# Optimization experiments

Measured on AMD Instinct MI355X. Metric: run time of the kernel, lower is better.

## Reference

```python
import jax, jax.numpy as jnp
import numpy as np
import math

B, S, D_MODEL, N_HEAD = 4, 2048, 1024, 16
D_K = D_MODEL // N_HEAD
ROPE_THETA = 10000.0


def _rope(x):
    # x: [B, H, S, Dk]; interleaved-pair rotary embedding.
    b, h, s, d = x.shape
    inv_freq = ROPE_THETA ** (-jnp.arange(0, d, 2, dtype=jnp.float32) / d)  # [d/2]
    ang = jnp.arange(s, dtype=jnp.float32)[:, None] * inv_freq[None, :]      # [S, d/2]
    cos, sin = jnp.cos(ang), jnp.sin(ang)
    x1, x2 = x[..., 0::2], x[..., 1::2]
    r1 = x1 * cos - x2 * sin
    r2 = x1 * sin + x2 * cos
    return jnp.stack([r1, r2], axis=-1).reshape(b, h, s, d)


def setup_inputs() -> dict:
    key = jax.random.key(0)
    ks = jax.random.split(key, 7)
    sc = 1.0 / math.sqrt(D_MODEL)
    return {
        "q": jax.random.normal(ks[0], (B, S, D_MODEL), jnp.float32),
        "k": jax.random.normal(ks[1], (B, S, D_MODEL), jnp.float32),
        "v": jax.random.normal(ks[2], (B, S, D_MODEL), jnp.float32),
        "Wq": jax.random.normal(ks[3], (D_MODEL, D_MODEL), jnp.float32) * sc,
        "Wk": jax.random.normal(ks[4], (D_MODEL, D_MODEL), jnp.float32) * sc,
        "Wv": jax.random.normal(ks[5], (D_MODEL, D_MODEL), jnp.float32) * sc,
        "Wo": jax.random.normal(ks[6], (D_MODEL, D_MODEL), jnp.float32) * sc,
    }


def _split(x):
    b, s, d = x.shape
    return x.reshape(b, s, N_HEAD, d // N_HEAD).transpose(0, 2, 1, 3)  # [B,H,S,Dk]


def reference(q, k, v, Wq, Wk, Wv, Wo):
    q = jnp.einsum("bsd,de->bse", q, Wq)
    k = jnp.einsum("bsd,de->bse", k, Wk)
    v = jnp.einsum("bsd,de->bse", v, Wv)
    qh, kh, vh = _split(q), _split(k), _split(v)
    qh, kh = _rope(qh), _rope(kh)
    scale = 1.0 / math.sqrt(D_K)
    score = jnp.einsum("bhqd,bhkd->bhqk", qh, kh) * scale  # [B,H,S,S]
    attn = jax.nn.softmax(score, axis=-1)
    out = jnp.einsum("bhqk,bhkd->bhqd", attn, vh)
    out = out.transpose(0, 2, 1, 3).reshape(q.shape[0], q.shape[1], D_MODEL)
    return jnp.einsum("bsd,de->bse", out, Wo)
```

## Files before the change

kernel.cpp:

```cpp
#include <hip/hip_runtime.h>
#include <stdint.h>

#define Bv 4
#define Sv 2048
#define Dv 1024
#define Hv 16
#define DKv 64
#define BSv (Bv * Sv)

typedef unsigned short u16;
typedef __attribute__((ext_vector_type(8))) short short8;
typedef __attribute__((ext_vector_type(8))) unsigned short u16x8;
typedef __attribute__((ext_vector_type(4))) unsigned short u16x4;
typedef __attribute__((ext_vector_type(4))) float f32x4;
typedef __attribute__((ext_vector_type(16))) float f32x16;

__device__ __forceinline__ u16 f2bf(float f) {
  union { float f; uint32_t u; } x; x.f = f;
  uint32_t r = x.u + 0x7FFFu + ((x.u >> 16) & 1u);
  return (u16)(r >> 16);
}

__device__ __forceinline__ void gl_lds16(const void* g, void* l) {
  __builtin_amdgcn_global_load_lds(
      (__attribute__((address_space(1))) void*)g,
      (__attribute__((address_space(3))) void*)l, 16, 0, 0);
}

__device__ __forceinline__ f32x4 mfma16(short8 a, short8 b, f32x4 c) {
  return __builtin_amdgcn_mfma_f32_16x16x32_bf16(a, b, c, 0, 0, 0);
}
__device__ __forceinline__ f32x16 mfma32(short8 a, short8 b, f32x16 c) {
  return __builtin_amdgcn_mfma_f32_32x32x16_bf16(a, b, c, 0, 0, 0);
}

__global__ __launch_bounds__(256) void conv_qkv(
    const float* __restrict__ q, const float* __restrict__ k,
    const float* __restrict__ v, u16* __restrict__ qb, u16* __restrict__ kb,
    u16* __restrict__ vb) {
  const float* src = (blockIdx.y == 0) ? q : (blockIdx.y == 1 ? k : v);
  u16* dst = (blockIdx.y == 0) ? qb : (blockIdx.y == 1 ? kb : vb);
  int i = (blockIdx.x * 256 + threadIdx.x) * 8;
  const float4* s4 = (const float4*)(src + i);
  float4 a = s4[0], b = s4[1];
  u16x8 o = { f2bf(a.x), f2bf(a.y), f2bf(a.z), f2bf(a.w),
              f2bf(b.x), f2bf(b.y), f2bf(b.z), f2bf(b.w) };
  *(u16x8*)(dst + i) = o;
}

__global__ __launch_bounds__(256) void conv_wt(
    const float* __restrict__ w0, const float* __restrict__ w1,
    const float* __restrict__ w2, const float* __restrict__ w3,
    u16* __restrict__ t0, u16* __restrict__ t1, u16* __restrict__ t2,
    u16* __restrict__ t3) {
  const float* W = (blockIdx.z == 0) ? w0 : (blockIdx.z == 1 ? w1 : (blockIdx.z == 2 ? w2 : w3));
  u16* T = (blockIdx.z == 0) ? t0 : (blockIdx.z == 1 ? t1 : (blockIdx.z == 2 ? t2 : t3));
  __shared__ u16 tile[64][72];
  int nb = blockIdx.x * 64, kb = blockIdx.y * 64;
  int t = threadIdx.x;
#pragma unroll
  for (int p = 0; p < 4; ++p) {
    int idx = p * 256 + t;
    int r = idx >> 4;
    int c4 = (idx & 15) * 4;
    float4 vv = *(const float4*)(W + (size_t)(kb + r) * Dv + nb + c4);
    tile[c4 + 0][r] = f2bf(vv.x);
    tile[c4 + 1][r] = f2bf(vv.y);
    tile[c4 + 2][r] = f2bf(vv.z);
    tile[c4 + 3][r] = f2bf(vv.w);
  }
  __syncthreads();
#pragma unroll
  for (int p = 0; p < 4; ++p) {
    int idx = p * 256 + t;
    int r = idx >> 4;
    int c4 = (idx & 15) * 4;
    u16x4 o = { tile[r][c4], tile[r][c4 + 1], tile[r][c4 + 2], tile[r][c4 + 3] };
    *(u16x4*)(T + (size_t)(nb + r) * Dv + kb + c4) = o;
  }
}

__global__ __launch_bounds__(256) void gemm_bt(
    const u16* __restrict__ A, const u16* __restrict__ Bt,
    void* __restrict__ Out, int mode) {
  __shared__ u16 As[128 * 64];
  __shared__ u16 Bs[128 * 64];
  int tid = threadIdx.x;
  int lane = tid & 63, wid = tid >> 6;
  int quad = lane >> 4, cc = lane & 15;
  int wm = (wid >> 1) * 64, wn = (wid & 1) * 64;
  int m0 = blockIdx.x * 128, n0 = blockIdx.y * 128;

  f32x4 acc[4][4];
#pragma unroll
  for (int mi = 0; mi < 4; ++mi)
#pragma unroll
    for (int ni = 0; ni < 4; ++ni) {
      f32x4 z = {0.f, 0.f, 0.f, 0.f};
      acc[mi][ni] = z;
    }

  for (int k0 = 0; k0 < Dv; k0 += 64) {
#pragma unroll
    for (int p = 0; p < 4; ++p) {
      int slot = p * 256 + tid;
      int row = slot >> 3, cl = slot & 7;
      int cg = cl ^ (row & 7);
      gl_lds16(A + (size_t)(m0 + row) * Dv + k0 + cg * 8, &As[slot * 8]);
    }
#pragma unroll
    for (int p = 0; p < 4; ++p) {
      int slot = p * 256 + tid;
      int row = slot >> 3, cl = slot & 7;
      int cg = cl ^ (row & 7);
      gl_lds16(Bt + (size_t)(n0 + row) * Dv + k0 + cg * 8, &Bs[slot * 8]);
    }
    __syncthreads();
#pragma unroll
    for (int kk = 0; kk < 2; ++kk) {
      short8 af[4], bf[4];
#pragma unroll
      for (int mi = 0; mi < 4; ++mi) {
        int row = wm + mi * 16 + cc;
        int cg = kk * 4 + quad;
        af[mi] = *(const short8*)&As[row * 64 + (cg ^ (row & 7)) * 8];
      }
#pragma unroll
      for (int ni = 0; ni < 4; ++ni) {
        int row = wn + ni * 16 + cc;
        int cg = kk * 4 + quad;
        bf[ni] = *(const short8*)&Bs[row * 64 + (cg ^ (row & 7)) * 8];
      }
#pragma unroll
      for (int mi = 0; mi < 4; ++mi)
#pragma unroll
        for (int ni = 0; ni < 4; ++ni)
          acc[mi][ni] = mfma16(af[mi], bf[ni], acc[mi][ni]);
    }
    __syncthreads();
  }

  if (mode <= 1) {
    u16* O = (u16*)Out;
    float postscale = (mode == 0) ? 0.18033688011112042f : 1.0f;
#pragma unroll
    for (int ni = 0; ni < 4; ++ni) {
      int n = n0 + wn + ni * 16 + cc;
      int h = n >> 6, d = n & 63;
      float inv = __expf(-(float)(d & 62) * (9.210340372f / 64.0f));
      float sign = (d & 1) ? 1.0f : -1.0f;
#pragma unroll
      for (int mi = 0; mi < 4; ++mi) {
        int mB = m0 + wm + mi * 16 + quad * 4;
#pragma unroll
        for (int r = 0; r < 4; ++r) {
          int m = mB + r;
          int b = m >> 11, s = m & (Sv - 1);
          float val = acc[mi][ni][r];
          float part = __shfl_xor(val, 1);
          float sn, cs;
          __sincosf((float)s * inv, &sn, &cs);
          float outv = (val * cs + sign * part * sn) * postscale;
          O[((size_t)(b * Hv + h) * Sv + s) * DKv + d] = f2bf(outv);
        }
      }
    }
  } else if (mode == 2) {
    u16* O = (u16*)Out;
#pragma unroll
    for (int ni = 0; ni < 4; ++ni) {
      int n = n0 + wn + ni * 16 + cc;
      int h = n >> 6, d = n & 63;
#pragma unroll
      for (int mi = 0; mi < 4; ++mi) {
        int mB = m0 + wm + mi * 16 + quad * 4;
        int b = mB >> 11, s = mB & (Sv - 1);
        u16x4 o4 = { f2bf(acc[mi][ni][0]), f2bf(acc[mi][ni][1]),
                     f2bf(acc[mi][ni][2]), f2bf(acc[mi][ni][3]) };
        *(u16x4*)&O[((size_t)(b * Hv + h) * DKv + d) * Sv + s] = o4;
      }
    }
  } else {
    float* O = (float*)Out;
#pragma unroll
    for (int ni = 0; ni < 4; ++ni) {
      int n = n0 + wn + ni * 16 + cc;
#pragma unroll
      for (int mi = 0; mi < 4; ++mi) {
        int mB = m0 + wm + mi * 16 + quad * 4;
#pragma unroll
        for (int r = 0; r < 4; ++r)
          O[(size_t)(mB + r) * Dv + n] = acc[mi][ni][r];
      }
    }
  }
}

__global__ __launch_bounds__(256, 2) void attn(
    const u16* __restrict__ Qp, const u16* __restrict__ Kp,
    const u16* __restrict__ Vt, u16* __restrict__ ctx) {
  __shared__ u16 Ks[2][64 * 64];
  __shared__ u16 Vs[2][64 * 64];
  __shared__ u16 Ps[4][32 * 64];
  int tid = threadIdx.x;
  int lane = tid & 63, wid = tid >> 6;
  int hi = lane >> 5, c32 = lane & 31;
  int sz = (c32 & 7) ^ ((c32 >> 3) & 3);
  int bh = blockIdx.y;
  int q0 = blockIdx.x * 256 + wid * 64;
  const u16* Qh = Qp + (size_t)bh * Sv * DKv;
  const u16* Kh = Kp + (size_t)bh * Sv * DKv;
  const u16* Vh = Vt + (size_t)bh * Sv * DKv;

  const short8 ones = { (short)0x3F80, (short)0x3F80, (short)0x3F80, (short)0x3F80,
                        (short)0x3F80, (short)0x3F80, (short)0x3F80, (short)0x3F80 };

  short8 qf[2][4];
#pragma unroll
  for (int qs = 0; qs < 2; ++qs)
#pragma unroll
    for (int kk = 0; kk < 4; ++kk)
      qf[qs][kk] = *(const short8*)&Qh[(size_t)(q0 + qs * 32 + c32) * DKv + kk * 16 + hi * 8];

  f32x16 o[2][2];
  f32x16 ol[2];
#pragma unroll
  for (int qs = 0; qs < 2; ++qs) {
#pragma unroll
    for (int dt = 0; dt < 2; ++dt)
#pragma unroll
      for (int r = 0; r < 16; ++r) o[qs][dt][r] = 0.f;
#pragma unroll
    for (int r = 0; r < 16; ++r) ol[qs][r] = 0.f;
  }

#pragma unroll
  for (int p = 0; p < 2; ++p) {
    int slot = p * 256 + tid;
    int row = slot >> 3, cl = slot & 7;
    int cg = cl ^ ((row & 7) ^ ((row >> 3) & 3));
    gl_lds16(Kh + (size_t)row * DKv + cg * 8, &Ks[0][slot * 8]);
    gl_lds16(Vh + (size_t)row * Sv + cg * 8, &Vs[0][slot * 8]);
  }

  for (int kt = 0; kt < Sv / 64; ++kt) {
    int cur = kt & 1;
    __syncthreads();

    if (kt + 1 < Sv / 64) {
      int s1 = (kt + 1) * 64;
#pragma unroll
      for (int p = 0; p < 2; ++p) {
        int slot = p * 256 + tid;
        int row = slot >> 3, cl = slot & 7;
        int cg = cl ^ ((row & 7) ^ ((row >> 3) & 3));
        gl_lds16(Kh + (size_t)(s1 + row) * DKv + cg * 8, &Ks[1 - cur][slot * 8]);
        gl_lds16(Vh + (size_t)row * Sv + s1 + cg * 8, &Vs[1 - cur][slot * 8]);
      }
    }

    short8 kf[2][4];
#pragma unroll
    for (int ks = 0; ks < 2; ++ks)
#pragma unroll
      for (int kk = 0; kk < 4; ++kk)
        kf[ks][kk] = *(const short8*)&Ks[cur][(ks * 32 + c32) * 64 + (((kk * 2 + hi) ^ sz)) * 8];

    short8 vf[2][4];

#pragma unroll
    for (int qs = 0; qs < 2; ++qs) {
      f32x16 st[2];
#pragma unroll
      for (int ks = 0; ks < 2; ++ks)
#pragma unroll
        for (int r = 0; r < 16; ++r) st[ks][r] = 0.f;
#pragma unroll
      for (int kk = 0; kk < 4; ++kk)
#pragma unroll
        for (int ks = 0; ks < 2; ++ks)
          st[ks] = mfma32(kf[ks][kk], qf[qs][kk], st[ks]);

#pragma unroll
      for (int ks = 0; ks < 2; ++ks)
#pragma unroll
        for (int g = 0; g < 4; ++g) {
          float e0 = __builtin_amdgcn_exp2f(st[ks][4 * g + 0]);
          float e1 = __builtin_amdgcn_exp2f(st[ks][4 * g + 1]);
          float e2 = __builtin_amdgcn_exp2f(st[ks][4 * g + 2]);
          float e3 = __builtin_amdgcn_exp2f(st[ks][4 * g + 3]);
          uint32_t w0 = __builtin_amdgcn_perm(__float_as_uint(e1), __float_as_uint(e0), 0x07060302u);
          uint32_t w1 = __builtin_amdgcn_perm(__float_as_uint(e3), __float_as_uint(e2), 0x07060302u);
          uint2 w = { w0, w1 };
          int ch = (ks * 4 + g) ^ sz;
          *(uint2*)&Ps[wid][c32 * 64 + ch * 8 + hi * 4] = w;
        }

      if (qs == 0) {
#pragma unroll
        for (int dt = 0; dt < 2; ++dt)
#pragma unroll
          for (int kk = 0; kk < 4; ++kk)
            vf[dt][kk] = *(const short8*)&Vs[cur][(dt * 32 + c32) * 64 + (((kk * 2 + hi) ^ sz)) * 8];
      }

#pragma unroll
      for (int kk = 0; kk < 4; ++kk) {
        short8 pf = *(const short8*)&Ps[wid][c32 * 64 + (((kk * 2 + hi) ^ sz)) * 8];
        ol[qs] = mfma32(pf, ones, ol[qs]);
        o[qs][0] = mfma32(pf, vf[0][kk], o[qs][0]);
        o[qs][1] = mfma32(pf, vf[1][kk], o[qs][1]);
      }
    }
  }

  int b = bh >> 4, h = bh & 15;
#pragma unroll
  for (int qs = 0; qs < 2; ++qs)
#pragma unroll
    for (int r = 0; r < 16; ++r) {
      int q = q0 + qs * 32 + (r & 3) + 8 * (r >> 2) + 4 * hi;
      float linv = 1.0f / ol[qs][r];
#pragma unroll
      for (int dt = 0; dt < 2; ++dt) {
        int d = h * DKv + dt * 32 + c32;
        ctx[((size_t)b * Sv + q) * Dv + d] = f2bf(o[qs][dt][r] * linv);
      }
    }
}

extern "C" void kernel_launch(void* const* d_in, const int* in_sizes, int n_in,
                              void* d_out, int out_size, void* d_ws, size_t ws_size,
                              hipStream_t stream) {
  (void)in_sizes; (void)n_in; (void)out_size; (void)ws_size;
  const float* q  = (const float*)d_in[0];
  const float* k  = (const float*)d_in[1];
  const float* v  = (const float*)d_in[2];
  const float* Wq = (const float*)d_in[3];
  const float* Wk = (const float*)d_in[4];
  const float* Wv = (const float*)d_in[5];
  const float* Wo = (const float*)d_in[6];

  char* ws = (char*)d_ws;
  size_t off = 0;
  const size_t big = (size_t)BSv * Dv * sizeof(u16);
  const size_t wsz = (size_t)Dv * Dv * sizeof(u16);
  u16* qb  = (u16*)(ws + off); off += big;
  u16* kb  = (u16*)(ws + off); off += big;
  u16* vb  = (u16*)(ws + off); off += big;
  u16* Wqt = (u16*)(ws + off); off += wsz;
  u16* Wkt = (u16*)(ws + off); off += wsz;
  u16* Wvt = (u16*)(ws + off); off += wsz;
  u16* Wot = (u16*)(ws + off); off += wsz;
  u16* Qp  = (u16*)(ws + off); off += big;
  u16* Kp  = (u16*)(ws + off); off += big;
  u16* Vtr = (u16*)(ws + off); off += big;
  u16* ctx = (u16*)(ws + off); off += big;

  conv_qkv<<<dim3(BSv * Dv / (256 * 8), 3), 256, 0, stream>>>(q, k, v, qb, kb, vb);
  conv_wt<<<dim3(Dv / 64, Dv / 64, 4), 256, 0, stream>>>(Wq, Wk, Wv, Wo, Wqt, Wkt, Wvt, Wot);
  gemm_bt<<<dim3(BSv / 128, Dv / 128), 256, 0, stream>>>(qb, Wqt, Qp, 0);
  gemm_bt<<<dim3(BSv / 128, Dv / 128), 256, 0, stream>>>(kb, Wkt, Kp, 1);
  gemm_bt<<<dim3(BSv / 128, Dv / 128), 256, 0, stream>>>(vb, Wvt, Vtr, 2);
  attn<<<dim3(Sv / 256, Bv * Hv), 256, 0, stream>>>(Qp, Kp, Vtr, ctx);
  gemm_bt<<<dim3(BSv / 128, Dv / 128), 256, 0, stream>>>(ctx, Wot, d_out, 3);
}
```

Before: 347.5 us.

## Use 32x32 MFMA in GEMMs, batch QKV projections, keep softmax P in registers

The projection GEMM switches from 16x16x32 to 32x32x16 bf16 MFMA tiles with a matching LDS swizzle. The three Q/K/V projections are merged into one launch using blockIdx.z. In attention, the P matrix is no longer staged through LDS: it is rearranged in registers with cross-half lane shuffles. The row sum is computed with scalar adds instead of an extra MFMA against a ones vector, and occupancy is raised to 3 blocks per SM. This removes LDS round-trips and a third of the attention MFMAs, at the cost of extra shuffles and VALU work.

After: 782.4 us. 2.25x slower.

```diff
diff --git a/kernel.cpp b/kernel.cpp
--- a/kernel.cpp
+++ b/kernel.cpp
@@ -12,7 +12,6 @@
 typedef __attribute__((ext_vector_type(8))) short short8;
 typedef __attribute__((ext_vector_type(8))) unsigned short u16x8;
 typedef __attribute__((ext_vector_type(4))) unsigned short u16x4;
-typedef __attribute__((ext_vector_type(4))) float f32x4;
 typedef __attribute__((ext_vector_type(16))) float f32x16;
 
 __device__ __forceinline__ u16 f2bf(float f) {
@@ -27,11 +26,12 @@
       (__attribute__((address_space(3))) void*)l, 16, 0, 0);
 }
 
-__device__ __forceinline__ f32x4 mfma16(short8 a, short8 b, f32x4 c) {
-  return __builtin_amdgcn_mfma_f32_16x16x32_bf16(a, b, c, 0, 0, 0);
-}
 __device__ __forceinline__ f32x16 mfma32(short8 a, short8 b, f32x16 c) {
   return __builtin_amdgcn_mfma_f32_32x32x16_bf16(a, b, c, 0, 0, 0);
+}
+
+__device__ __forceinline__ float trsum(uint32_t w) {
+  return __uint_as_float(w & 0xFFFF0000u) + __uint_as_float(w << 16);
 }
 
 __global__ __launch_bounds__(256) void conv_qkv(
@@ -81,61 +81,63 @@
 }
 
 __global__ __launch_bounds__(256) void gemm_bt(
-    const u16* __restrict__ A, const u16* __restrict__ Bt,
-    void* __restrict__ Out, int mode) {
+    const u16* __restrict__ A0, const u16* __restrict__ A1, const u16* __restrict__ A2,
+    const u16* __restrict__ B0, const u16* __restrict__ B1, const u16* __restrict__ B2,
+    void* __restrict__ O0, void* __restrict__ O1, void* __restrict__ O2,
+    int modeSel) {
   __shared__ u16 As[128 * 64];
   __shared__ u16 Bs[128 * 64];
+  int z = blockIdx.z;
+  const u16* A  = (z == 0) ? A0 : (z == 1 ? A1 : A2);
+  const u16* Bt = (z == 0) ? B0 : (z == 1 ? B1 : B2);
+  void* Out     = (z == 0) ? O0 : (z == 1 ? O1 : O2);
+  int mode = (modeSel < 0) ? z : modeSel;
+
   int tid = threadIdx.x;
   int lane = tid & 63, wid = tid >> 6;
-  int quad = lane >> 4, cc = lane & 15;
+  int hi = lane >> 5, c32 = lane & 31;
+  int sz = (c32 & 7) ^ ((c32 >> 3) & 3);
   int wm = (wid >> 1) * 64, wn = (wid & 1) * 64;
   int m0 = blockIdx.x * 128, n0 = blockIdx.y * 128;
 
-  f32x4 acc[4][4];
-#pragma unroll
-  for (int mi = 0; mi < 4; ++mi)
-#pragma unroll
-    for (int ni = 0; ni < 4; ++ni) {
-      f32x4 z = {0.f, 0.f, 0.f, 0.f};
-      acc[mi][ni] = z;
-    }
+  f32x16 acc[2][2];
+#pragma unroll
+  for (int mi = 0; mi < 2; ++mi)
+#pragma unroll
+    for (int ni = 0; ni < 2; ++ni)
+#pragma unroll
+      for (int r = 0; r < 16; ++r) acc[mi][ni][r] = 0.f;
 
   for (int k0 = 0; k0 < Dv; k0 += 64) {
 #pragma unroll
     for (int p = 0; p < 4; ++p) {
       int slot = p * 256 + tid;
       int row = slot >> 3, cl = slot & 7;
-      int cg = cl ^ (row & 7);
+      int cg = cl ^ ((row & 7) ^ ((row >> 3) & 3));
       gl_lds16(A + (size_t)(m0 + row) * Dv + k0 + cg * 8, &As[slot * 8]);
     }
 #pragma unroll
     for (int p = 0; p < 4; ++p) {
       int slot = p * 256 + tid;
       int row = slot >> 3, cl = slot & 7;
-      int cg = cl ^ (row & 7);
+      int cg = cl ^ ((row & 7) ^ ((row >> 3) & 3));
       gl_lds16(Bt + (size_t)(n0 + row) * Dv + k0 + cg * 8, &Bs[slot * 8]);
     }
     __syncthreads();
 #pragma unroll
-    for (int kk = 0; kk < 2; ++kk) {
-      short8 af[4], bf[4];
-#pragma unroll
-      for (int mi = 0; mi < 4; ++mi) {
-        int row = wm + mi * 16 + cc;
-        int cg = kk * 4 + quad;
-        af[mi] = *(const short8*)&As[row * 64 + (cg ^ (row & 7)) * 8];
-      }
-#pragma unroll
-      for (int ni = 0; ni < 4; ++ni) {
-        int row = wn + ni * 16 + cc;
-        int cg = kk * 4 + quad;
-        bf[ni] = *(const short8*)&Bs[row * 64 + (cg ^ (row & 7)) * 8];
-      }
-#pragma unroll
-      for (int mi = 0; mi < 4; ++mi)
-#pragma unroll
-        for (int ni = 0; ni < 4; ++ni)
-          acc[mi][ni] = mfma16(af[mi], bf[ni], acc[mi][ni]);
+    for (int dk = 0; dk < 4; ++dk) {
+      short8 af[2], bf[2];
+#pragma unroll
+      for (int mi = 0; mi < 2; ++mi)
+        af[mi] = *(const short8*)&As[(wm + mi * 32 + c32) * 64 + (((dk * 2 + hi) ^ sz)) * 8];
+#pragma unroll
+      for (int ni = 0; ni < 2; ++ni)
+        bf[ni] = *(const short8*)&Bs[(wn + ni * 32 + c32) * 64 + (((dk * 2 + hi) ^ sz)) * 8];
+#pragma unroll
+      for (int mi = 0; mi < 2; ++mi)
+#pragma unroll
+        for (int ni = 0; ni < 2; ++ni)
+          acc[mi][ni] = mfma32(af[mi], bf[ni], acc[mi][ni]);
     }
     __syncthreads();
   }
@@ -144,17 +146,17 @@
     u16* O = (u16*)Out;
     float postscale = (mode == 0) ? 0.18033688011112042f : 1.0f;
 #pragma unroll
-    for (int ni = 0; ni < 4; ++ni) {
-      int n = n0 + wn + ni * 16 + cc;
+    for (int ni = 0; ni < 2; ++ni) {
+      int n = n0 + wn + ni * 32 + c32;
       int h = n >> 6, d = n & 63;
       float inv = __expf(-(float)(d & 62) * (9.210340372f / 64.0f));
       float sign = (d & 1) ? 1.0f : -1.0f;
 #pragma unroll
-      for (int mi = 0; mi < 4; ++mi) {
-        int mB = m0 + wm + mi * 16 + quad * 4;
-#pragma unroll
-        for (int r = 0; r < 4; ++r) {
-          int m = mB + r;
+      for (int mi = 0; mi < 2; ++mi) {
+        int mB = m0 + wm + mi * 32;
+#pragma unroll
+        for (int r = 0; r < 16; ++r) {
+          int m = mB + (r & 3) + 8 * (r >> 2) + 4 * hi;
           int b = m >> 11, s = m & (Sv - 1);
           float val = acc[mi][ni][r];
           float part = __shfl_xor(val, 1);
@@ -168,40 +170,44 @@
   } else if (mode == 2) {
     u16* O = (u16*)Out;
 #pragma unroll
-    for (int ni = 0; ni < 4; ++ni) {
-      int n = n0 + wn + ni * 16 + cc;
+    for (int ni = 0; ni < 2; ++ni) {
+      int n = n0 + wn + ni * 32 + c32;
       int h = n >> 6, d = n & 63;
 #pragma unroll
-      for (int mi = 0; mi < 4; ++mi) {
-        int mB = m0 + wm + mi * 16 + quad * 4;
-        int b = mB >> 11, s = mB & (Sv - 1);
-        u16x4 o4 = { f2bf(acc[mi][ni][0]), f2bf(acc[mi][ni][1]),
-                     f2bf(acc[mi][ni][2]), f2bf(acc[mi][ni][3]) };
-        *(u16x4*)&O[((size_t)(b * Hv + h) * DKv + d) * Sv + s] = o4;
+      for (int mi = 0; mi < 2; ++mi) {
+        int mB = m0 + wm + mi * 32;
+#pragma unroll
+        for (int g = 0; g < 4; ++g) {
+          int sbase = mB + 8 * g + 4 * hi;
+          int b = sbase >> 11, s = sbase & (Sv - 1);
+          u16x4 o4 = { f2bf(acc[mi][ni][4 * g + 0]), f2bf(acc[mi][ni][4 * g + 1]),
+                       f2bf(acc[mi][ni][4 * g + 2]), f2bf(acc[mi][ni][4 * g + 3]) };
+          *(u16x4*)&O[((size_t)(b * Hv + h) * DKv + d) * Sv + s] = o4;
+        }
       }
     }
   } else {
     float* O = (float*)Out;
 #pragma unroll
-    for (int ni = 0; ni < 4; ++ni) {
-      int n = n0 + wn + ni * 16 + cc;
-#pragma unroll
-      for (int mi = 0; mi < 4; ++mi) {
-        int mB = m0 + wm + mi * 16 + quad * 4;
-#pragma unroll
-        for (int r = 0; r < 4; ++r)
-          O[(size_t)(mB + r) * Dv + n] = acc[mi][ni][r];
-      }
-    }
-  }
-}
-
-__global__ __launch_bounds__(256, 2) void attn(
+    for (int ni = 0; ni < 2; ++ni) {
+      int n = n0 + wn + ni * 32 + c32;
+#pragma unroll
+      for (int mi = 0; mi < 2; ++mi) {
+        int mB = m0 + wm + mi * 32;
+#pragma unroll
+        for (int r = 0; r < 16; ++r)
+          O[(size_t)(mB + (r & 3) + 8 * (r >> 2) + 4 * hi) * Dv + n] = acc[mi][ni][r];
+      }
+    }
+  }
+}
+
+__global__ __launch_bounds__(256, 3) void attn(
     const u16* __restrict__ Qp, const u16* __restrict__ Kp,
     const u16* __restrict__ Vt, u16* __restrict__ ctx) {
   __shared__ u16 Ks[2][64 * 64];
   __shared__ u16 Vs[2][64 * 64];
-  __shared__ u16 Ps[4][32 * 64];
+  __shared__ float Lb[4][2][32];
   int tid = threadIdx.x;
   int lane = tid & 63, wid = tid >> 6;
   int hi = lane >> 5, c32 = lane & 31;
@@ -212,27 +218,21 @@
   const u16* Kh = Kp + (size_t)bh * Sv * DKv;
   const u16* Vh = Vt + (size_t)bh * Sv * DKv;
 
-  const short8 ones = { (short)0x3F80, (short)0x3F80, (short)0x3F80, (short)0x3F80,
-                        (short)0x3F80, (short)0x3F80, (short)0x3F80, (short)0x3F80 };
-
   short8 qf[2][4];
 #pragma unroll
   for (int qs = 0; qs < 2; ++qs)
 #pragma unroll
-    for (int kk = 0; kk < 4; ++kk)
-      qf[qs][kk] = *(const short8*)&Qh[(size_t)(q0 + qs * 32 + c32) * DKv + kk * 16 + hi * 8];
+    for (int dk = 0; dk < 4; ++dk)
+      qf[qs][dk] = *(const short8*)&Qh[(size_t)(q0 + qs * 32 + c32) * DKv + dk * 16 + hi * 8];
 
   f32x16 o[2][2];
-  f32x16 ol[2];
-#pragma unroll
-  for (int qs = 0; qs < 2; ++qs) {
+  float lacc[2] = {0.f, 0.f};
+#pragma unroll
+  for (int qs = 0; qs < 2; ++qs)
 #pragma unroll
     for (int dt = 0; dt < 2; ++dt)
 #pragma unroll
       for (int r = 0; r < 16; ++r) o[qs][dt][r] = 0.f;
-#pragma unroll
-    for (int r = 0; r < 16; ++r) ol[qs][r] = 0.f;
-  }
 
 #pragma unroll
   for (int p = 0; p < 2; ++p) {
@@ -259,68 +259,67 @@
       }
     }
 
-    short8 kf[2][4];
-#pragma unroll
-    for (int ks = 0; ks < 2; ++ks)
-#pragma unroll
-      for (int kk = 0; kk < 4; ++kk)
-        kf[ks][kk] = *(const short8*)&Ks[cur][(ks * 32 + c32) * 64 + (((kk * 2 + hi) ^ sz)) * 8];
-
-    short8 vf[2][4];
-
 #pragma unroll
     for (int qs = 0; qs < 2; ++qs) {
-      f32x16 st[2];
-#pragma unroll
-      for (int ks = 0; ks < 2; ++ks)
-#pragma unroll
-        for (int r = 0; r < 16; ++r) st[ks][r] = 0.f;
-#pragma unroll
-      for (int kk = 0; kk < 4; ++kk)
-#pragma unroll
-        for (int ks = 0; ks < 2; ++ks)
-          st[ks] = mfma32(kf[ks][kk], qf[qs][kk], st[ks]);
-
-#pragma unroll
-      for (int ks = 0; ks < 2; ++ks)
-#pragma unroll
-        for (int g = 0; g < 4; ++g) {
-          float e0 = __builtin_amdgcn_exp2f(st[ks][4 * g + 0]);
-          float e1 = __builtin_amdgcn_exp2f(st[ks][4 * g + 1]);
-          float e2 = __builtin_amdgcn_exp2f(st[ks][4 * g + 2]);
-          float e3 = __builtin_amdgcn_exp2f(st[ks][4 * g + 3]);
-          uint32_t w0 = __builtin_amdgcn_perm(__float_as_uint(e1), __float_as_uint(e0), 0x07060302u);
-          uint32_t w1 = __builtin_amdgcn_perm(__float_as_uint(e3), __float_as_uint(e2), 0x07060302u);
-          uint2 w = { w0, w1 };
-          int ch = (ks * 4 + g) ^ sz;
-          *(uint2*)&Ps[wid][c32 * 64 + ch * 8 + hi * 4] = w;
+#pragma unroll
+      for (int half = 0; half < 2; ++half) {
+        f32x16 st;
+#pragma unroll
+        for (int r = 0; r < 16; ++r) st[r] = 0.f;
+#pragma unroll
+        for (int dk = 0; dk < 4; ++dk) {
+          short8 kfv = *(const short8*)&Ks[cur][(half * 32 + c32) * 64 + (((dk * 2 + hi) ^ sz)) * 8];
+          st = mfma32(kfv, qf[qs][dk], st);
         }
-
-      if (qs == 0) {
-#pragma unroll
-        for (int dt = 0; dt < 2; ++dt)
-#pragma unroll
-          for (int kk = 0; kk < 4; ++kk)
-            vf[dt][kk] = *(const short8*)&Vs[cur][(dt * 32 + c32) * 64 + (((kk * 2 + hi) ^ sz)) * 8];
-      }
-
-#pragma unroll
-      for (int kk = 0; kk < 4; ++kk) {
-        short8 pf = *(const short8*)&Ps[wid][c32 * 64 + (((kk * 2 + hi) ^ sz)) * 8];
-        ol[qs] = mfma32(pf, ones, ol[qs]);
-        o[qs][0] = mfma32(pf, vf[0][kk], o[qs][0]);
-        o[qs][1] = mfma32(pf, vf[1][kk], o[qs][1]);
-      }
-    }
-  }
-
+#pragma unroll
+        for (int pp = 0; pp < 2; ++pp) {
+          int pk = half * 2 + pp;
+          int ggo = (2 * pk + hi) & 3;
+          int ggs = (2 * pk + 1 - hi) & 3;
+          float a0 = __builtin_amdgcn_exp2f(st[4 * ggo + 0]);
+          float a1 = __builtin_amdgcn_exp2f(st[4 * ggo + 1]);
+          float a2 = __builtin_amdgcn_exp2f(st[4 * ggo + 2]);
+          float a3 = __builtin_amdgcn_exp2f(st[4 * ggo + 3]);
+          float b0 = __builtin_amdgcn_exp2f(st[4 * ggs + 0]);
+          float b1 = __builtin_amdgcn_exp2f(st[4 * ggs + 1]);
+          float b2 = __builtin_amdgcn_exp2f(st[4 * ggs + 2]);
+          float b3 = __builtin_amdgcn_exp2f(st[4 * ggs + 3]);
+          uint32_t ow0 = __builtin_amdgcn_perm(__float_as_uint(a1), __float_as_uint(a0), 0x07060302u);
+          uint32_t ow1 = __builtin_amdgcn_perm(__float_as_uint(a3), __float_as_uint(a2), 0x07060302u);
+          uint32_t sw0 = __builtin_amdgcn_perm(__float_as_uint(b1), __float_as_uint(b0), 0x07060302u);
+          uint32_t sw1 = __builtin_amdgcn_perm(__float_as_uint(b3), __float_as_uint(b2), 0x07060302u);
+          lacc[qs] += (trsum(ow0) + trsum(ow1)) + (trsum(sw0) + trsum(sw1));
+          uint32_t r0 = (uint32_t)__shfl_xor((int)sw0, 32);
+          uint32_t r1 = (uint32_t)__shfl_xor((int)sw1, 32);
+          union { uint32_t u[4]; short8 s8; } pu;
+          pu.u[0] = hi ? r0 : ow0;
+          pu.u[1] = hi ? r1 : ow1;
+          pu.u[2] = hi ? ow0 : r0;
+          pu.u[3] = hi ? ow1 : r1;
+#pragma unroll
+          for (int dt = 0; dt < 2; ++dt) {
+            short8 vf = *(const short8*)&Vs[cur][(dt * 32 + c32) * 64 + (((pk * 2 + hi) ^ sz)) * 8];
+            o[qs][dt] = mfma32(pu.s8, vf, o[qs][dt]);
+          }
+        }
+      }
+    }
+  }
+
+#pragma unroll
+  for (int qs = 0; qs < 2; ++qs) {
+    lacc[qs] += __shfl_xor(lacc[qs], 32);
+    Lb[wid][qs][c32] = lacc[qs];
+  }
+  __syncthreads();
   int b = bh >> 4, h = bh & 15;
 #pragma unroll
   for (int qs = 0; qs < 2; ++qs)
 #pragma unroll
     for (int r = 0; r < 16; ++r) {
-      int q = q0 + qs * 32 + (r & 3) + 8 * (r >> 2) + 4 * hi;
-      float linv = 1.0f / ol[qs][r];
+      int ql = (r & 3) + 8 * (r >> 2) + 4 * hi;
+      int q = q0 + qs * 32 + ql;
+      float linv = 1.0f / Lb[wid][qs][ql];
 #pragma unroll
       for (int dt = 0; dt < 2; ++dt) {
         int d = h * DKv + dt * 32 + c32;
@@ -359,9 +358,9 @@
 
   conv_qkv<<<dim3(BSv * Dv / (256 * 8), 3), 256, 0, stream>>>(q, k, v, qb, kb, vb);
   conv_wt<<<dim3(Dv / 64, Dv / 64, 4), 256, 0, stream>>>(Wq, Wk, Wv, Wo, Wqt, Wkt, Wvt, Wot);
-  gemm_bt<<<dim3(BSv / 128, Dv / 128), 256, 0, stream>>>(qb, Wqt, Qp, 0);
-  gemm_bt<<<dim3(BSv / 128, Dv / 128), 256, 0, stream>>>(kb, Wkt, Kp, 1);
-  gemm_bt<<<dim3(BSv / 128, Dv / 128), 256, 0, stream>>>(vb, Wvt, Vtr, 2);
+  gemm_bt<<<dim3(BSv / 128, Dv / 128, 3), 256, 0, stream>>>(
+      qb, kb, vb, Wqt, Wkt, Wvt, Qp, Kp, Vtr, -1);
   attn<<<dim3(Sv / 256, Bv * Hv), 256, 0, stream>>>(Qp, Kp, Vtr, ctx);
-  gemm_bt<<<dim3(BSv / 128, Dv / 128), 256, 0, stream>>>(ctx, Wot, d_out, 3);
-}
+  gemm_bt<<<dim3(BSv / 128, Dv / 128, 1), 256, 0, stream>>>(
+      ctx, ctx, ctx, Wot, Wot, Wot, d_out, d_out, d_out, 3);
+}
```
